# Kernel optimization log

Measured on AMD Instinct MI355X. Metric: run time of the kernel, lower is better.

Reference implementation:

```python
import jax, jax.numpy as jnp
import numpy as np

N_NODES = 50000
N_EDGES = 800000
D_FEAT = 128
D_EDGE = 64
N_HEADS = 4
OUT_DIM = 32
HID = N_HEADS * OUT_DIM  # 128


def segment_softmax(logits, seg, num_segments):
    # jraph.segment_softmax: subtract per-segment max, exp, normalize by per-segment sum
    seg_max = jax.ops.segment_max(logits, seg, num_segments=num_segments)
    e = jnp.exp(logits - seg_max[seg])
    denom = jax.ops.segment_sum(e, seg, num_segments=num_segments)
    return e / denom[seg]


def setup_inputs() -> dict:
    key = jax.random.key(0)
    ks = jax.random.split(key, 12)
    s = 1.0 / np.sqrt(D_FEAT)
    se = 1.0 / np.sqrt(D_EDGE)
    return {
        "nodes": jax.random.normal(ks[0], (N_NODES, D_FEAT), jnp.float32),
        "edges": jax.random.normal(ks[1], (N_EDGES, D_EDGE), jnp.float32),
        "senders": jax.random.randint(ks[2], (N_EDGES,), 0, N_NODES, jnp.int32),
        "receivers": jax.random.randint(ks[3], (N_EDGES,), 0, N_NODES, jnp.int32),
        "Wq": jax.random.normal(ks[4], (D_FEAT, HID), jnp.float32) * s,
        "bq": jnp.zeros((HID,), jnp.float32),
        "Wk": jax.random.normal(ks[5], (D_FEAT, HID), jnp.float32) * s,
        "bk": jnp.zeros((HID,), jnp.float32),
        "Wv": jax.random.normal(ks[6], (D_FEAT, HID), jnp.float32) * s,
        "bv": jnp.zeros((HID,), jnp.float32),
        "We": jax.random.normal(ks[7], (D_EDGE, HID), jnp.float32) * se,
        "Wu": jax.random.normal(ks[8], (D_FEAT, OUT_DIM), jnp.float32) * s,
        "bu": jnp.zeros((OUT_DIM,), jnp.float32),
    }


def reference(nodes, edges, senders, receivers, Wq, bq, Wk, bk, Wv, bv, We, Wu, bu):
    n_nodes = nodes.shape[0]
    send_feats = nodes[senders]    # [E, D]
    recv_feats = nodes[receivers]  # [E, D]

    q = (recv_feats @ Wq + bq).reshape(-1, N_HEADS, OUT_DIM)
    k = (send_feats @ Wk + bk).reshape(-1, N_HEADS, OUT_DIM)
    v = (send_feats @ Wv + bv).reshape(-1, N_HEADS, OUT_DIM)
    e = (edges @ We).reshape(-1, N_HEADS, OUT_DIM)

    attn = (q * k).sum(-1) / jnp.sqrt(jnp.asarray(OUT_DIM, q.dtype))  # [E, H]
    attn = segment_softmax(attn, receivers, n_nodes)                  # [E, H]

    msgs = (attn[:, :, None] * (v + e)).mean(axis=1)                  # [E, OUT_DIM]
    aggr = jax.ops.segment_sum(msgs, receivers, num_segments=n_nodes) # [N, OUT_DIM]

    feats = nodes @ Wu + bu
    return jax.nn.relu(feats + aggr)
```

## Files before the change

### kernel.cpp

```cpp
#include <hip/hip_runtime.h>
#include <math.h>

#define N_NODES 50000
#define N_EDGES 800000
#define D_FEAT 128
#define D_EDGE 64
#define HID 128
#define OUT_DIM 32

typedef unsigned short u16;
typedef short bf16x8 __attribute__((ext_vector_type(8)));
typedef float f32x4 __attribute__((ext_vector_type(4)));

__device__ __forceinline__ u16 f2bf(float x) {
    unsigned u = __float_as_uint(x);
    unsigned r = (u >> 16) & 1u;
    return (u16)((u + 0x7FFFu + r) >> 16);
}
__device__ __forceinline__ float bf2f(u16 s) { return __uint_as_float(((unsigned)s) << 16); }
__device__ __forceinline__ float bflo(unsigned u) { return __uint_as_float(u << 16); }
__device__ __forceinline__ float bfhi(unsigned u) { return __uint_as_float(u & 0xFFFF0000u); }

__device__ __forceinline__ float dot16(uint4 a, uint4 b) {
    float s = 0.f;
    s += bflo(a.x) * bflo(b.x) + bfhi(a.x) * bfhi(b.x);
    s += bflo(a.y) * bflo(b.y) + bfhi(a.y) * bfhi(b.y);
    s += bflo(a.z) * bflo(b.z) + bfhi(a.z) * bfhi(b.z);
    s += bflo(a.w) * bflo(b.w) + bfhi(a.w) * bfhi(b.w);
    return s;
}

__global__ void zero_i32(int* __restrict__ p, int n) {
    int i = blockIdx.x * 256 + threadIdx.x;
    if (i < n) p[i] = 0;
}

__global__ void prep_weights(const float* __restrict__ Wq, const float* __restrict__ Wk,
                             const float* __restrict__ Wv, const float* __restrict__ We,
                             const float* __restrict__ Wu,
                             u16* __restrict__ WT_all, u16* __restrict__ WeTg) {
    int id = blockIdx.x * 256 + threadIdx.x;
    if (id < 49152) {
        int m = id >> 14, rem = id & 16383;
        int c = rem >> 7, k = rem & 127;
        const float* W = (m == 0) ? Wq : (m == 1) ? Wk : Wv;
        WT_all[id] = f2bf(W[k * HID + c]);
    } else if (id < 57344) {
        int j = id - 49152;
        int c = j >> 6, k = j & 63;
        WeTg[j] = f2bf(We[k * HID + c]);
    } else {
        int j = id - 57344;
        int c = j >> 7, k = j & 127;
        WT_all[49152 + j] = f2bf(Wu[k * OUT_DIM + c]);
    }
}

__global__ __launch_bounds__(256) void node_qkv_v3(
    const float* __restrict__ nodes, const u16* __restrict__ WT_all,
    const float* __restrict__ bq, const float* __restrict__ bk, const float* __restrict__ bv,
    const float* __restrict__ bu,
    u16* __restrict__ Q, u16* __restrict__ Kk, u16* __restrict__ Vp,
    float* __restrict__ baseout)
{
    __shared__ __align__(16) u16 Alds[4][32 * 136];

    const int tid = threadIdx.x;
    const int wave = tid >> 6, lane = tid & 63;
    const int quad = lane >> 4, l15 = lane & 15;
    const int rowbase = blockIdx.x * 128 + wave * 32;

    u16* As = &Alds[wave][0];
    #pragma unroll
    for (int it = 0; it < 16; ++it) {
        int idx = lane + it * 64;
        int row = idx >> 5, k4 = (idx & 31) * 4;
        float4 v = make_float4(0.f, 0.f, 0.f, 0.f);
        if (rowbase + row < N_NODES)
            v = *(const float4*)&nodes[(size_t)(rowbase + row) * D_FEAT + k4];
        ushort4 b;
        b.x = f2bf(v.x); b.y = f2bf(v.y); b.z = f2bf(v.z); b.w = f2bf(v.w);
        *(ushort4*)&As[row * 136 + k4] = b;
    }

    bf16x8 afr[2][4];
    #pragma unroll
    for (int rt = 0; rt < 2; ++rt)
        #pragma unroll
        for (int ks = 0; ks < 4; ++ks)
            afr[rt][ks] = *(const bf16x8*)&As[(rt * 16 + l15) * 136 + ks * 32 + quad * 8];

    #pragma unroll
    for (int m = 0; m < 3; ++m) {
        const u16* WT = WT_all + (size_t)m * 16384;
        const float* bvec = (m == 0) ? bq : (m == 1) ? bk : bv;
        u16* C = (m == 0) ? Q : (m == 1) ? Kk : Vp;

        f32x4 acc[2][8];
        #pragma unroll
        for (int rt = 0; rt < 2; ++rt)
            #pragma unroll
            for (int ct = 0; ct < 8; ++ct)
                acc[rt][ct] = (f32x4){0.f, 0.f, 0.f, 0.f};

        #pragma unroll
        for (int ks = 0; ks < 4; ++ks) {
            #pragma unroll
            for (int ct = 0; ct < 8; ++ct) {
                bf16x8 b = *(const bf16x8*)&WT[(ct * 16 + l15) * 128 + ks * 32 + quad * 8];
                acc[0][ct] = __builtin_amdgcn_mfma_f32_16x16x32_bf16(afr[0][ks], b, acc[0][ct], 0, 0, 0);
                acc[1][ct] = __builtin_amdgcn_mfma_f32_16x16x32_bf16(afr[1][ks], b, acc[1][ct], 0, 0, 0);
            }
        }

        #pragma unroll
        for (int ct = 0; ct < 8; ++ct) {
            int cbase = ct * 16 + l15;
            float bias = bvec[cbase];
            int oidx = (m == 2) ? ((cbase & 31) * 4 + (cbase >> 5)) : cbase;
            #pragma unroll
            for (int rt = 0; rt < 2; ++rt)
                #pragma unroll
                for (int r = 0; r < 4; ++r) {
                    int n = rowbase + rt * 16 + quad * 4 + r;
                    if (n < N_NODES)
                        C[(size_t)n * HID + oidx] = f2bf(acc[rt][ct][r] + bias);
                }
        }
    }

    {
        const u16* WuT = WT_all + 49152;
        f32x4 accu[2][2];
        #pragma unroll
        for (int rt = 0; rt < 2; ++rt)
            #pragma unroll
            for (int ct = 0; ct < 2; ++ct)
                accu[rt][ct] = (f32x4){0.f, 0.f, 0.f, 0.f};
        #pragma unroll
        for (int ks = 0; ks < 4; ++ks) {
            #pragma unroll
            for (int ct = 0; ct < 2; ++ct) {
                bf16x8 b = *(const bf16x8*)&WuT[(ct * 16 + l15) * 128 + ks * 32 + quad * 8];
                accu[0][ct] = __builtin_amdgcn_mfma_f32_16x16x32_bf16(afr[0][ks], b, accu[0][ct], 0, 0, 0);
                accu[1][ct] = __builtin_amdgcn_mfma_f32_16x16x32_bf16(afr[1][ks], b, accu[1][ct], 0, 0, 0);
            }
        }
        #pragma unroll
        for (int ct = 0; ct < 2; ++ct) {
            int cbase = ct * 16 + l15;
            float bias = bu[cbase];
            #pragma unroll
            for (int rt = 0; rt < 2; ++rt)
                #pragma unroll
                for (int r = 0; r < 4; ++r) {
                    int n = rowbase + rt * 16 + quad * 4 + r;
                    if (n < N_NODES)
                        baseout[(size_t)n * OUT_DIM + cbase] = accu[rt][ct][r] + bias;
                }
        }
    }
}

__global__ void hist_kernel(const int* __restrict__ receivers, int* __restrict__ count) {
    int e = blockIdx.x * 256 + threadIdx.x;
    atomicAdd(&count[receivers[e]], 1);
}

__global__ __launch_bounds__(256) void scan1(const int* __restrict__ count,
                                             int* __restrict__ incl, int* __restrict__ bsum) {
    __shared__ int sh[256];
    int gid = blockIdx.x * 256 + threadIdx.x;
    int v = (gid < N_NODES) ? count[gid] : 0;
    sh[threadIdx.x] = v; __syncthreads();
    #pragma unroll
    for (int off = 1; off < 256; off <<= 1) {
        int t = (threadIdx.x >= off) ? sh[threadIdx.x - off] : 0;
        __syncthreads();
        sh[threadIdx.x] += t;
        __syncthreads();
    }
    if (gid < N_NODES) incl[gid] = sh[threadIdx.x];
    if (threadIdx.x == 255) bsum[blockIdx.x] = sh[255];
}

__global__ __launch_bounds__(256) void scan2(const int* __restrict__ bsum,
                                             int* __restrict__ boff, int nblocks) {
    __shared__ int sh[256];
    int v = (threadIdx.x < nblocks) ? bsum[threadIdx.x] : 0;
    sh[threadIdx.x] = v; __syncthreads();
    #pragma unroll
    for (int off = 1; off < 256; off <<= 1) {
        int t = (threadIdx.x >= off) ? sh[threadIdx.x - off] : 0;
        __syncthreads();
        sh[threadIdx.x] += t;
        __syncthreads();
    }
    boff[threadIdx.x] = sh[threadIdx.x] - v;
}

__global__ __launch_bounds__(256) void scan3(const int* __restrict__ incl,
                                             const int* __restrict__ count,
                                             const int* __restrict__ boff,
                                             int* __restrict__ startp, int* __restrict__ cursor) {
    int gid = blockIdx.x * 256 + threadIdx.x;
    if (gid < N_NODES) {
        int ex = incl[gid] - count[gid] + boff[blockIdx.x];
        startp[gid] = ex;
        cursor[gid] = ex;
    }
    if (gid == 0) startp[N_NODES] = N_EDGES;
}

__global__ void scatter_v5(const int* __restrict__ senders, const int* __restrict__ receivers,
                           int* __restrict__ cursor, int* __restrict__ sorted,
                           int* __restrict__ ssend) {
    int e = blockIdx.x * 256 + threadIdx.x;
    int r = receivers[e];
    int s = senders[e];
    int pos = atomicAdd(&cursor[r], 1);
    sorted[pos] = e;
    ssend[pos] = s;
}

__global__ __launch_bounds__(256) void node_softmax(
    const u16* __restrict__ Q, const u16* __restrict__ K,
    const int* __restrict__ startp, const int* __restrict__ sorted,
    const int* __restrict__ ssend, float* __restrict__ wspill,
    float* __restrict__ wnorm)
{
    const int wid = (blockIdx.x * 256 + threadIdx.x) >> 6;
    const int lane = threadIdx.x & 63;
    const int h = lane & 3, el = lane >> 2;
    const int s0 = startp[wid];
    const int deg = startp[wid + 1] - s0;
    if (deg == 0) return;
    const int nc = (deg + 15) >> 4;
    const float sc = 0.17677669529663687f;

    const uint4* qp = (const uint4*)&Q[(size_t)wid * HID + h * 32];
    const uint4 q0 = qp[0], q1 = qp[1], q2 = qp[2], q3 = qp[3];

    float expv0 = 0.f, expv1 = 0.f, expv2 = 0.f, expv3 = 0.f, expv4 = 0.f, expv5 = 0.f;
    float dtot = 0.f;

    #pragma unroll
    for (int c = 0; c < 6; ++c) {
        if (c >= nc) break;
        int sl = c * 16 + el;
        float w = 0.f;
        if (sl < deg) {
            int s = ssend[s0 + sl];
            const uint4* kp = (const uint4*)&K[(size_t)s * HID + h * 32];
            float a = dot16(q0, kp[0]) + dot16(q1, kp[1])
                    + dot16(q2, kp[2]) + dot16(q3, kp[3]);
            w = expf(a * sc);
        }
        if (c == 0) expv0 = w; else if (c == 1) expv1 = w; else if (c == 2) expv2 = w;
        else if (c == 3) expv3 = w; else if (c == 4) expv4 = w; else expv5 = w;
        float t = w;
        t += __shfl_xor(t, 4); t += __shfl_xor(t, 8);
        t += __shfl_xor(t, 16); t += __shfl_xor(t, 32);
        dtot += t;
    }
    for (int c = 6; c < nc; ++c) {
        int sl = c * 16 + el;
        float w = 0.f;
        if (sl < deg) {
            int s = ssend[s0 + sl];
            const uint4* kp = (const uint4*)&K[(size_t)s * HID + h * 32];
            float a = dot16(q0, kp[0]) + dot16(q1, kp[1])
                    + dot16(q2, kp[2]) + dot16(q3, kp[3]);
            w = expf(a * sc);
            wspill[(size_t)(s0 + sl) * 4 + h] = w;
        }
        float t = w;
        t += __shfl_xor(t, 4); t += __shfl_xor(t, 8);
        t += __shfl_xor(t, 16); t += __shfl_xor(t, 32);
        dtot += t;
    }

    const float inv = 0.25f / dtot;

    #pragma unroll
    for (int c = 0; c < 6; ++c) {
        if (c >= nc) break;
        int sl = c * 16 + el;
        if (sl < deg) {
            float w = (c == 0) ? expv0 : (c == 1) ? expv1 : (c == 2) ? expv2
                    : (c == 3) ? expv3 : (c == 4) ? expv4 : expv5;
            int e = sorted[s0 + sl];
            wnorm[(size_t)e * 4 + h] = w * inv;
        }
    }
    if (nc > 6) {
        asm volatile("s_waitcnt vmcnt(0)" ::: "memory");
        for (int c = 6; c < nc; ++c) {
            int sl = c * 16 + el;
            if (sl < deg) {
                float w = wspill[(size_t)(s0 + sl) * 4 + h];
                int e = sorted[s0 + sl];
                wnorm[(size_t)e * 4 + h] = w * inv;
            }
        }
    }
}

__global__ __launch_bounds__(256) void edge_messages_v9(
    const float* __restrict__ edges, const u16* __restrict__ WeTg,
    const u16* __restrict__ Vp, const float* __restrict__ wnorm,
    const int* __restrict__ senders, u16* __restrict__ msg)
{
    __shared__ __align__(16) u16 Ae[4][32 * 72];

    const int tid = threadIdx.x;
    const int wave = tid >> 6, lane = tid & 63;
    const int quad = lane >> 4, l15 = lane & 15;
    const int base = blockIdx.x * 128 + wave * 32;

    int snd8[8];
    float w8[8][4];
    #pragma unroll
    for (int idx = 0; idx < 8; ++idx) {
        int el = base + (idx >> 2) * 16 + quad * 4 + (idx & 3);
        snd8[idx] = senders[el];
        float4 w = *(const float4*)&wnorm[(size_t)el * 4];
        w8[idx][0] = w.x; w8[idx][1] = w.y; w8[idx][2] = w.z; w8[idx][3] = w.w;
    }

    u16* As = &Ae[wave][0];
    #pragma unroll
    for (int it = 0; it < 8; ++it) {
        int idx = lane + it * 64;
        int row = idx >> 4, k4 = (idx & 15) * 4;
        float4 v = *(const float4*)&edges[(size_t)(base + row) * D_EDGE + k4];
        ushort4 b;
        b.x = f2bf(v.x); b.y = f2bf(v.y); b.z = f2bf(v.z); b.w = f2bf(v.w);
        *(ushort4*)&As[row * 72 + k4] = b;
    }

    bf16x8 afr[2][2];
    #pragma unroll
    for (int rt = 0; rt < 2; ++rt)
        #pragma unroll
        for (int ks = 0; ks < 2; ++ks)
            afr[rt][ks] = *(const bf16x8*)&As[(rt * 16 + l15) * 72 + ks * 32 + quad * 8];

    #pragma unroll
    for (int p = 0; p < 2; ++p) {
        const int d = p * 16 + l15;
        ushort4 vp8[8];
        #pragma unroll
        for (int idx = 0; idx < 8; ++idx)
            vp8[idx] = *(const ushort4*)&Vp[(size_t)snd8[idx] * HID + d * 4];

        f32x4 acc[2][4];
        #pragma unroll
        for (int rt = 0; rt < 2; ++rt)
            #pragma unroll
            for (int c = 0; c < 4; ++c)
                acc[rt][c] = (f32x4){0.f, 0.f, 0.f, 0.f};

        #pragma unroll
        for (int ks = 0; ks < 2; ++ks) {
            #pragma unroll
            for (int c = 0; c < 4; ++c) {
                bf16x8 b = *(const bf16x8*)&WeTg[((2 * c + p) * 16 + l15) * 64 + ks * 32 + quad * 8];
                acc[0][c] = __builtin_amdgcn_mfma_f32_16x16x32_bf16(afr[0][ks], b, acc[0][c], 0, 0, 0);
                acc[1][c] = __builtin_amdgcn_mfma_f32_16x16x32_bf16(afr[1][ks], b, acc[1][c], 0, 0, 0);
            }
        }

        #pragma unroll
        for (int idx = 0; idx < 8; ++idx) {
            int rt = idx >> 2, r = idx & 3;
            int el = base + rt * 16 + quad * 4 + r;
            float out = w8[idx][0] * (acc[rt][0][r] + bf2f(vp8[idx].x))
                      + w8[idx][1] * (acc[rt][1][r] + bf2f(vp8[idx].y))
                      + w8[idx][2] * (acc[rt][2][r] + bf2f(vp8[idx].z))
                      + w8[idx][3] * (acc[rt][3][r] + bf2f(vp8[idx].w));
            msg[(size_t)el * OUT_DIM + d] = f2bf(out);
        }
    }
}

__global__ __launch_bounds__(256) void aggregate4(
    const u16* __restrict__ msg, const float* __restrict__ baseout,
    const int* __restrict__ sorted, const int* __restrict__ startp,
    float* __restrict__ out)
{
    int id = blockIdx.x * 256 + threadIdx.x;
    int n = id >> 5, d = id & 31;
    float acc = baseout[id];
    int s = startp[n], e = startp[n + 1];
    for (int i = s; i < e; ++i) {
        int el = sorted[i];
        acc += bf2f(msg[(size_t)el * OUT_DIM + d]);
    }
    out[id] = fmaxf(acc, 0.f);
}

extern "C" void kernel_launch(void* const* d_in, const int* in_sizes, int n_in,
                              void* d_out, int out_size, void* d_ws, size_t ws_size,
                              hipStream_t stream) {
    const float* nodes     = (const float*)d_in[0];
    const float* edges     = (const float*)d_in[1];
    const int*   senders   = (const int*)d_in[2];
    const int*   receivers = (const int*)d_in[3];
    const float* Wq = (const float*)d_in[4];
    const float* bq = (const float*)d_in[5];
    const float* Wk = (const float*)d_in[6];
    const float* bk = (const float*)d_in[7];
    const float* Wv = (const float*)d_in[8];
    const float* bv = (const float*)d_in[9];
    const float* We = (const float*)d_in[10];
    const float* Wu = (const float*)d_in[11];
    const float* bu = (const float*)d_in[12];
    float* out = (float*)d_out;

    char* p = (char*)d_ws;
    u16* Qb    = (u16*)p; p += (size_t)N_NODES * HID * 2;
    u16* Kb    = (u16*)p; p += (size_t)N_NODES * HID * 2;
    u16* Vperm = (u16*)p; p += (size_t)N_NODES * HID * 2;
    u16* WT_all= (u16*)p; p += (size_t)(3 * HID * HID + OUT_DIM * HID) * 2;
    u16* WeTg  = (u16*)p; p += (size_t)HID * D_EDGE * 2;
    float* wspill = (float*)p; p += (size_t)N_EDGES * 4 * 4;
    float* wnorm  = (float*)p; p += (size_t)N_EDGES * 4 * 4;
    u16* msg   = (u16*)p; p += (size_t)N_EDGES * OUT_DIM * 2;
    float* baseout = (float*)p; p += (size_t)N_NODES * OUT_DIM * 4;
    int* count  = (int*)p; p += (size_t)N_NODES * 4;
    int* incl   = (int*)p; p += (size_t)N_NODES * 4;
    int* startp = (int*)p; p += (size_t)(N_NODES + 4) * 4;
    int* cursor = (int*)p; p += (size_t)N_NODES * 4;
    int* sorted = (int*)p; p += (size_t)N_EDGES * 4;
    int* ssend  = (int*)p; p += (size_t)N_EDGES * 4;
    int* bsum   = (int*)p; p += 256 * 4;
    int* boff   = (int*)p; p += 256 * 4;

    const int SCAN_BLOCKS = (N_NODES + 255) / 256;

    hipLaunchKernelGGL(zero_i32, dim3(SCAN_BLOCKS), dim3(256), 0, stream, count, N_NODES);
    hipLaunchKernelGGL(hist_kernel, dim3(N_EDGES / 256), dim3(256), 0, stream,
                       receivers, count);
    hipLaunchKernelGGL(scan1, dim3(SCAN_BLOCKS), dim3(256), 0, stream, count, incl, bsum);
    hipLaunchKernelGGL(scan2, dim3(1), dim3(256), 0, stream, bsum, boff, SCAN_BLOCKS);
    hipLaunchKernelGGL(scan3, dim3(SCAN_BLOCKS), dim3(256), 0, stream,
                       incl, count, boff, startp, cursor);
    hipLaunchKernelGGL(scatter_v5, dim3(N_EDGES / 256), dim3(256), 0, stream,
                       senders, receivers, cursor, sorted, ssend);
    hipLaunchKernelGGL(prep_weights, dim3(61440 / 256), dim3(256), 0, stream,
                       Wq, Wk, Wv, We, Wu, WT_all, WeTg);
    hipLaunchKernelGGL(node_qkv_v3, dim3((N_NODES + 127) / 128), dim3(256), 0, stream,
                       nodes, WT_all, bq, bk, bv, bu, Qb, Kb, Vperm, baseout);
    hipLaunchKernelGGL(node_softmax, dim3(N_NODES / 4), dim3(256), 0, stream,
                       Qb, Kb, startp, sorted, ssend, wspill, wnorm);
    hipLaunchKernelGGL(edge_messages_v9, dim3(N_EDGES / 128), dim3(256), 0, stream,
                       edges, WeTg, Vperm, wnorm, senders, msg);
    hipLaunchKernelGGL(aggregate4, dim3(N_NODES * OUT_DIM / 256), dim3(256), 0, stream,
                       msg, baseout, sorted, startp, out);
}
```

Measured before the change: 604.7 us.

## Load MFMA A-fragments directly from global, repack V for 16-byte gathers, unroll aggregate

Node and edge GEMM kernels now load fp32 rows straight into registers as bf16 MFMA fragments, dropping the LDS staging buffers and their store/load round trip. V is written in a new permuted layout so each edge-message lane gathers all eight values it needs with one 16-byte load, issued early before the weight loads. The aggregation loop is unrolled by two to keep more independent gathers in flight. Direct global fragment loads are less coalesced than the old cooperative row loads, which may raise memory transactions.

```diff
diff --git a/kernel.cpp b/kernel.cpp
--- a/kernel.cpp
+++ b/kernel.cpp
@@ -56,39 +56,40 @@
     }
 }
 
-__global__ __launch_bounds__(256) void node_qkv_v3(
+__global__ __launch_bounds__(256) void node_qkv_v4(
     const float* __restrict__ nodes, const u16* __restrict__ WT_all,
     const float* __restrict__ bq, const float* __restrict__ bk, const float* __restrict__ bv,
     const float* __restrict__ bu,
     u16* __restrict__ Q, u16* __restrict__ Kk, u16* __restrict__ Vp,
     float* __restrict__ baseout)
 {
-    __shared__ __align__(16) u16 Alds[4][32 * 136];
-
     const int tid = threadIdx.x;
     const int wave = tid >> 6, lane = tid & 63;
     const int quad = lane >> 4, l15 = lane & 15;
     const int rowbase = blockIdx.x * 128 + wave * 32;
 
-    u16* As = &Alds[wave][0];
-    #pragma unroll
-    for (int it = 0; it < 16; ++it) {
-        int idx = lane + it * 64;
-        int row = idx >> 5, k4 = (idx & 31) * 4;
-        float4 v = make_float4(0.f, 0.f, 0.f, 0.f);
-        if (rowbase + row < N_NODES)
-            v = *(const float4*)&nodes[(size_t)(rowbase + row) * D_FEAT + k4];
-        ushort4 b;
-        b.x = f2bf(v.x); b.y = f2bf(v.y); b.z = f2bf(v.z); b.w = f2bf(v.w);
-        *(ushort4*)&As[row * 136 + k4] = b;
-    }
-
     bf16x8 afr[2][4];
     #pragma unroll
-    for (int rt = 0; rt < 2; ++rt)
-        #pragma unroll
-        for (int ks = 0; ks < 4; ++ks)
-            afr[rt][ks] = *(const bf16x8*)&As[(rt * 16 + l15) * 136 + ks * 32 + quad * 8];
+    for (int rt = 0; rt < 2; ++rt) {
+        int row = rowbase + rt * 16 + l15;
+        bool ok = row < N_NODES;
+        const float* rp = &nodes[(size_t)row * D_FEAT];
+        #pragma unroll
+        for (int ks = 0; ks < 4; ++ks) {
+            float4 v0 = make_float4(0.f, 0.f, 0.f, 0.f);
+            float4 v1 = make_float4(0.f, 0.f, 0.f, 0.f);
+            if (ok) {
+                v0 = *(const float4*)(rp + ks * 32 + quad * 8);
+                v1 = *(const float4*)(rp + ks * 32 + quad * 8 + 4);
+            }
+            bf16x8 a;
+            a[0] = (short)f2bf(v0.x); a[1] = (short)f2bf(v0.y);
+            a[2] = (short)f2bf(v0.z); a[3] = (short)f2bf(v0.w);
+            a[4] = (short)f2bf(v1.x); a[5] = (short)f2bf(v1.y);
+            a[6] = (short)f2bf(v1.z); a[7] = (short)f2bf(v1.w);
+            afr[rt][ks] = a;
+        }
+    }
 
     #pragma unroll
     for (int m = 0; m < 3; ++m) {
@@ -117,7 +118,11 @@
         for (int ct = 0; ct < 8; ++ct) {
             int cbase = ct * 16 + l15;
             float bias = bvec[cbase];
-            int oidx = (m == 2) ? ((cbase & 31) * 4 + (cbase >> 5)) : cbase;
+            int oidx = cbase;
+            if (m == 2) {
+                int h = cbase >> 5, d = cbase & 31;
+                oidx = (d & 15) * 8 + (d >> 4) * 4 + h;
+            }
             #pragma unroll
             for (int rt = 0; rt < 2; ++rt)
                 #pragma unroll
@@ -306,53 +311,55 @@
     }
 }
 
-__global__ __launch_bounds__(256) void edge_messages_v9(
+__global__ __launch_bounds__(256) void edge_messages_v11(
     const float* __restrict__ edges, const u16* __restrict__ WeTg,
-    const u16* __restrict__ Vp, const float* __restrict__ wnorm,
+    const u16* __restrict__ Vp2, const float* __restrict__ wnorm,
     const int* __restrict__ senders, u16* __restrict__ msg)
 {
-    __shared__ __align__(16) u16 Ae[4][32 * 72];
-
     const int tid = threadIdx.x;
     const int wave = tid >> 6, lane = tid & 63;
     const int quad = lane >> 4, l15 = lane & 15;
     const int base = blockIdx.x * 128 + wave * 32;
 
     int snd8[8];
-    float w8[8][4];
     #pragma unroll
     for (int idx = 0; idx < 8; ++idx) {
         int el = base + (idx >> 2) * 16 + quad * 4 + (idx & 3);
         snd8[idx] = senders[el];
+    }
+    uint4 vpg[8];
+    #pragma unroll
+    for (int idx = 0; idx < 8; ++idx)
+        vpg[idx] = *(const uint4*)&Vp2[(size_t)snd8[idx] * HID + l15 * 8];
+
+    float w8[8][4];
+    #pragma unroll
+    for (int idx = 0; idx < 8; ++idx) {
+        int el = base + (idx >> 2) * 16 + quad * 4 + (idx & 3);
         float4 w = *(const float4*)&wnorm[(size_t)el * 4];
         w8[idx][0] = w.x; w8[idx][1] = w.y; w8[idx][2] = w.z; w8[idx][3] = w.w;
     }
 
-    u16* As = &Ae[wave][0];
-    #pragma unroll
-    for (int it = 0; it < 8; ++it) {
-        int idx = lane + it * 64;
-        int row = idx >> 4, k4 = (idx & 15) * 4;
-        float4 v = *(const float4*)&edges[(size_t)(base + row) * D_EDGE + k4];
-        ushort4 b;
-        b.x = f2bf(v.x); b.y = f2bf(v.y); b.z = f2bf(v.z); b.w = f2bf(v.w);
-        *(ushort4*)&As[row * 72 + k4] = b;
-    }
-
     bf16x8 afr[2][2];
     #pragma unroll
-    for (int rt = 0; rt < 2; ++rt)
-        #pragma unroll
-        for (int ks = 0; ks < 2; ++ks)
-            afr[rt][ks] = *(const bf16x8*)&As[(rt * 16 + l15) * 72 + ks * 32 + quad * 8];
+    for (int rt = 0; rt < 2; ++rt) {
+        const float* rp = &edges[(size_t)(base + rt * 16 + l15) * D_EDGE];
+        #pragma unroll
+        for (int ks = 0; ks < 2; ++ks) {
+            float4 v0 = *(const float4*)(rp + ks * 32 + quad * 8);
+            float4 v1 = *(const float4*)(rp + ks * 32 + quad * 8 + 4);
+            bf16x8 a;
+            a[0] = (short)f2bf(v0.x); a[1] = (short)f2bf(v0.y);
+            a[2] = (short)f2bf(v0.z); a[3] = (short)f2bf(v0.w);
+            a[4] = (short)f2bf(v1.x); a[5] = (short)f2bf(v1.y);
+            a[6] = (short)f2bf(v1.z); a[7] = (short)f2bf(v1.w);
+            afr[rt][ks] = a;
+        }
+    }
 
     #pragma unroll
     for (int p = 0; p < 2; ++p) {
         const int d = p * 16 + l15;
-        ushort4 vp8[8];
-        #pragma unroll
-        for (int idx = 0; idx < 8; ++idx)
-            vp8[idx] = *(const ushort4*)&Vp[(size_t)snd8[idx] * HID + d * 4];
 
         f32x4 acc[2][4];
         #pragma unroll
@@ -375,16 +382,18 @@
         for (int idx = 0; idx < 8; ++idx) {
             int rt = idx >> 2, r = idx & 3;
             int el = base + rt * 16 + quad * 4 + r;
-            float out = w8[idx][0] * (acc[rt][0][r] + bf2f(vp8[idx].x))
-                      + w8[idx][1] * (acc[rt][1][r] + bf2f(vp8[idx].y))
-                      + w8[idx][2] * (acc[rt][2][r] + bf2f(vp8[idx].z))
-                      + w8[idx][3] * (acc[rt][3][r] + bf2f(vp8[idx].w));
+            unsigned d0 = p ? vpg[idx].z : vpg[idx].x;
+            unsigned d1 = p ? vpg[idx].w : vpg[idx].y;
+            float out = w8[idx][0] * (acc[rt][0][r] + bflo(d0))
+                      + w8[idx][1] * (acc[rt][1][r] + bfhi(d0))
+                      + w8[idx][2] * (acc[rt][2][r] + bflo(d1))
+                      + w8[idx][3] * (acc[rt][3][r] + bfhi(d1));
             msg[(size_t)el * OUT_DIM + d] = f2bf(out);
         }
     }
 }
 
-__global__ __launch_bounds__(256) void aggregate4(
+__global__ __launch_bounds__(256) void aggregate5(
     const u16* __restrict__ msg, const float* __restrict__ baseout,
     const int* __restrict__ sorted, const int* __restrict__ startp,
     float* __restrict__ out)
@@ -393,10 +402,15 @@
     int n = id >> 5, d = id & 31;
     float acc = baseout[id];
     int s = startp[n], e = startp[n + 1];
-    for (int i = s; i < e; ++i) {
-        int el = sorted[i];
-        acc += bf2f(msg[(size_t)el * OUT_DIM + d]);
-    }
+    int i = s;
+    for (; i + 1 < e; i += 2) {
+        int e0 = sorted[i], e1 = sorted[i + 1];
+        float m0 = bf2f(msg[(size_t)e0 * OUT_DIM + d]);
+        float m1 = bf2f(msg[(size_t)e1 * OUT_DIM + d]);
+        acc += m0 + m1;
+    }
+    if (i < e)
+        acc += bf2f(msg[(size_t)sorted[i] * OUT_DIM + d]);
     out[id] = fmaxf(acc, 0.f);
 }
 
@@ -450,12 +464,12 @@
                        senders, receivers, cursor, sorted, ssend);
     hipLaunchKernelGGL(prep_weights, dim3(61440 / 256), dim3(256), 0, stream,
                        Wq, Wk, Wv, We, Wu, WT_all, WeTg);
-    hipLaunchKernelGGL(node_qkv_v3, dim3((N_NODES + 127) / 128), dim3(256), 0, stream,
+    hipLaunchKernelGGL(node_qkv_v4, dim3((N_NODES + 127) / 128), dim3(256), 0, stream,
                        nodes, WT_all, bq, bk, bv, bu, Qb, Kb, Vperm, baseout);
     hipLaunchKernelGGL(node_softmax, dim3(N_NODES / 4), dim3(256), 0, stream,
                        Qb, Kb, startp, sorted, ssend, wspill, wnorm);
-    hipLaunchKernelGGL(edge_messages_v9, dim3(N_EDGES / 128), dim3(256), 0, stream,
+    hipLaunchKernelGGL(edge_messages_v11, dim3(N_EDGES / 128), dim3(256), 0, stream,
                        edges, WeTg, Vperm, wnorm, senders, msg);
-    hipLaunchKernelGGL(aggregate4, dim3(N_NODES * OUT_DIM / 256), dim3(256), 0, stream,
+    hipLaunchKernelGGL(aggregate5, dim3(N_NODES * OUT_DIM / 256), dim3(256), 0, stream,
                        msg, baseout, sorted, startp, out);
 }
```

After: 586.4 us. 1.03x faster.
